# Kernel optimization log

Hardware: AMD Instinct MI355X
Metric: run time of the kernel (lower is better)

## Reference

```python
import jax, jax.numpy as jnp
import numpy as np

EMBED_DIM = 4096
NUM_HEADS = 32
HEAD_DIM = EMBED_DIM // NUM_HEADS  # 128
KV_LEN = 8192


def setup_inputs() -> dict:
    key = jax.random.key(0)
    ks = jax.random.split(key, 12)
    s = 1.0 / np.sqrt(EMBED_DIM)
    return {
        "x": jax.random.normal(ks[0], (EMBED_DIM,), jnp.float32),
        "v": jax.random.normal(ks[1], (KV_LEN, NUM_HEADS, HEAD_DIM), jnp.float32),
        "k": jax.random.normal(ks[2], (KV_LEN, NUM_HEADS, HEAD_DIM), jnp.float32),
        "Wv": jax.random.normal(ks[3], (EMBED_DIM, EMBED_DIM), jnp.float32) * s,
        "bv": jnp.zeros((EMBED_DIM,), jnp.float32),
        "Wq": jax.random.normal(ks[4], (EMBED_DIM, EMBED_DIM), jnp.float32) * s,
        "bq": jnp.zeros((EMBED_DIM,), jnp.float32),
        "Wk": jax.random.normal(ks[5], (EMBED_DIM, EMBED_DIM), jnp.float32) * s,
        "bk": jnp.zeros((EMBED_DIM,), jnp.float32),
        "Wo": jax.random.normal(ks[6], (EMBED_DIM, EMBED_DIM), jnp.float32) * s,
        "bo": jnp.zeros((EMBED_DIM,), jnp.float32),
    }


def reference(x, v, k, Wv, bv, Wq, bq, Wk, bk, Wo, bo):
    # Project the single incoming token to q/k/v heads.
    v_i = (x @ Wv + bv).reshape(1, NUM_HEADS, HEAD_DIM)
    q_i = (x @ Wq + bq).reshape(NUM_HEADS, HEAD_DIM)
    k_i = (x @ Wk + bk).reshape(1, NUM_HEADS, HEAD_DIM)
    # Rolling cache: drop oldest slot, append new token.
    v = jnp.concatenate((v[1:], v_i), axis=0)  # [KV_LEN, H, D]
    k = jnp.concatenate((k[1:], k_i), axis=0)
    # Valid slots are those with any nonzero value entry.
    mask = jnp.any(v != 0, axis=(1, 2))  # [KV_LEN]
    attn = jnp.einsum('hd,khd->hk', q_i, k) / jnp.sqrt(jnp.float32(HEAD_DIM))
    attn = jnp.where(mask, attn, -jnp.inf)
    attn = jax.nn.softmax(attn, axis=-1)  # [H, KV_LEN]
    values = jnp.einsum('hk,khd->hd', attn, v).reshape(EMBED_DIM)
    out_i = values @ Wo + bo
    return (out_i, v, k)
```

## Files before the change

### kernel.cpp

```cpp
#include <hip/hip_runtime.h>

#define E 4096
#define H 32
#define L 8192
#define SCALE 0.08838834764831845f

#define WS_QACC 0
#define WS_KACC 16384
#define WS_VACC 32768
#define WS_OACC 49152
#define WS_NUMP 53248
#define WS_DENP 118784
#define WS_NUM  119808
#define WS_DEN  123904
#define WS_ZERO_FLOATS 123968

typedef float fv4 __attribute__((ext_vector_type(4)));

__device__ __forceinline__ fv4 ntload4(const float* p) {
  return __builtin_nontemporal_load(reinterpret_cast<const fv4*>(p));
}
__device__ __forceinline__ void ntstore4(float* p, fv4 v) {
  __builtin_nontemporal_store(v, reinterpret_cast<fv4*>(p));
}

__global__ __launch_bounds__(256) void zero_ws(float* __restrict__ ws) {
  int i = blockIdx.x * 256 + threadIdx.x;
  if (i < WS_ZERO_FLOATS) ws[i] = 0.f;
}

__global__ __launch_bounds__(256) void gemv_qkv(const float* __restrict__ x,
    const float* __restrict__ Wq, const float* __restrict__ Wk,
    const float* __restrict__ Wv, float* __restrict__ ws) {
  int b = blockIdx.x;
  int mat = b >> 7;
  int rem = b & 127;
  int chunk = rem >> 2;
  int g = rem & 3;
  const float* W = (mat == 0) ? Wq : (mat == 1) ? Wk : Wv;
  int rep = (b >> 2) & 3;
  float* acc = ws + ((mat == 0) ? WS_QACC : (mat == 1) ? WS_KACC : WS_VACC)
                  + (rep << 12);
  int t = threadIdx.x;
  int j = (g << 10) + (t << 2);
  float ax = 0.f, ay = 0.f, az = 0.f, aw = 0.f;
  int i0 = chunk << 7;
  #pragma unroll 8
  for (int r = 0; r < 128; ++r) {
    int i = i0 + r;
    float xi = x[i];
    const fv4 w4 = ntload4(W + (size_t)i * E + j);
    ax += xi * w4.x; ay += xi * w4.y; az += xi * w4.z; aw += xi * w4.w;
  }
  atomicAdd(acc + j + 0, ax);
  atomicAdd(acc + j + 1, ay);
  atomicAdd(acc + j + 2, az);
  atomicAdd(acc + j + 3, aw);
}

#define SLOTS 16
__device__ __forceinline__ void load_slot(int o, int t,
    const float* __restrict__ kin, const float* __restrict__ vin,
    const float* __restrict__ ws, const float* __restrict__ bk,
    const float* __restrict__ bv, fv4 k4[4], fv4 v4[4]) {
  if (o < L - 1) {
    const float* ks = kin + (size_t)(o + 1) * E;
    const float* vs = vin + (size_t)(o + 1) * E;
    #pragma unroll
    for (int c = 0; c < 4; ++c) {
      int e = (c << 10) + (t << 2);
      k4[c] = ntload4(ks + e);
      v4[c] = ntload4(vs + e);
    }
  } else {
    #pragma unroll
    for (int c = 0; c < 4; ++c) {
      int e = (c << 10) + (t << 2);
      fv4 ka = *reinterpret_cast<const fv4*>(ws + WS_KACC + e);
      fv4 va = *reinterpret_cast<const fv4*>(ws + WS_VACC + e);
      #pragma unroll
      for (int r = 1; r < 4; ++r) {
        ka += *reinterpret_cast<const fv4*>(ws + WS_KACC + (r << 12) + e);
        va += *reinterpret_cast<const fv4*>(ws + WS_VACC + (r << 12) + e);
      }
      k4[c] = ka + *reinterpret_cast<const fv4*>(bk + e);
      v4[c] = va + *reinterpret_cast<const fv4*>(bv + e);
    }
  }
}

__global__ __launch_bounds__(256) void kvpass(const float* __restrict__ kin,
    const float* __restrict__ vin,
    const float* __restrict__ bq, const float* __restrict__ bk,
    const float* __restrict__ bv,
    float* __restrict__ kout, float* __restrict__ vout,
    float* __restrict__ ws) {
  __shared__ float wlds[SLOTS * 32];
  __shared__ int flags[SLOTS];
  int t = threadIdx.x;
  if (t < SLOTS) flags[t] = 0;
  fv4 q4[4];
  #pragma unroll
  for (int c = 0; c < 4; ++c) {
    int e = (c << 10) + (t << 2);
    fv4 qa = *reinterpret_cast<const fv4*>(ws + WS_QACC + e);
    #pragma unroll
    for (int r = 1; r < 4; ++r)
      qa += *reinterpret_cast<const fv4*>(ws + WS_QACC + (r << 12) + e);
    q4[c] = qa + *reinterpret_cast<const fv4*>(bq + e);
  }
  __syncthreads();

  float accx[4] = {0,0,0,0}, accy[4] = {0,0,0,0};
  float accz[4] = {0,0,0,0}, accw[4] = {0,0,0,0};
  int base = blockIdx.x * SLOTS;
  int rep = blockIdx.x & 15;

  fv4 kc[4], vc[4], kn[4], vn[4];
  load_slot(base, t, kin, vin, ws, bk, bv, kc, vc);

  for (int s = 0; s < SLOTS; ++s) {
    int o = base + s;
    if (s + 1 < SLOTS)
      load_slot(o + 1, t, kin, vin, ws, bk, bv, kn, vn);
    float* kd = kout + (size_t)o * E;
    float* vd = vout + (size_t)o * E;
    #pragma unroll
    for (int c = 0; c < 4; ++c) {
      int e = (c << 10) + (t << 2);
      ntstore4(kd + e, kc[c]);
      ntstore4(vd + e, vc[c]);
    }
    bool nz = false;
    #pragma unroll
    for (int c = 0; c < 4; ++c) {
      float pp = kc[c].x * q4[c].x + kc[c].y * q4[c].y +
                 kc[c].z * q4[c].z + kc[c].w * q4[c].w;
      #pragma unroll
      for (int off = 16; off >= 1; off >>= 1)
        pp += __shfl_xor(pp, off);
      float w = __expf(pp * SCALE);
      accx[c] += w * vc[c].x; accy[c] += w * vc[c].y;
      accz[c] += w * vc[c].z; accw[c] += w * vc[c].w;
      if ((t & 31) == 0) wlds[(s << 5) + (c << 3) + (t >> 5)] = w;
      nz = nz || vc[c].x != 0.f || vc[c].y != 0.f || vc[c].z != 0.f || vc[c].w != 0.f;
    }
    unsigned long long b = __ballot(nz);
    if ((t & 63) == 0 && b != 0ULL) atomicOr(&flags[s], 1);
    #pragma unroll
    for (int c = 0; c < 4; ++c) { kc[c] = kn[c]; vc[c] = vn[c]; }
  }
  float* num = ws + WS_NUMP + (rep << 12);
  #pragma unroll
  for (int c = 0; c < 4; ++c) {
    int e = (c << 10) + (t << 2);
    atomicAdd(num + e + 0, accx[c]);
    atomicAdd(num + e + 1, accy[c]);
    atomicAdd(num + e + 2, accz[c]);
    atomicAdd(num + e + 3, accw[c]);
  }
  __syncthreads();
  if (t < 32) {
    float d = 0.f;
    #pragma unroll
    for (int s = 0; s < SLOTS; ++s)
      if (flags[s]) d += wlds[(s << 5) + t];
    atomicAdd(ws + WS_DENP + (rep << 6) + t, d);
  }
}

__global__ __launch_bounds__(256) void merge(float* __restrict__ ws) {
  int e = blockIdx.x * 256 + threadIdx.x;
  float s = 0.f;
  #pragma unroll
  for (int r = 0; r < 16; ++r) s += ws[WS_NUMP + (r << 12) + e];
  ws[WS_NUM + e] = s;
  if (e < 64) {
    float d = 0.f;
    #pragma unroll
    for (int r = 0; r < 16; ++r) d += ws[WS_DENP + (r << 6) + e];
    ws[WS_DEN + e] = d;
  }
}

__global__ __launch_bounds__(256) void gemv_out(const float* __restrict__ Wo,
    const float* __restrict__ bo, float* __restrict__ ws) {
  int b = blockIdx.x;
  int chunk = b >> 2;
  int g = b & 3;
  int t = threadIdx.x;
  int j = (g << 10) + (t << 2);
  const float* num = ws + WS_NUM;
  const float* den = ws + WS_DEN;
  __shared__ float vals[64];
  int i0 = chunk << 6;
  if (t < 64) vals[t] = num[i0 + t] / den[(i0 + t) >> 7];
  __syncthreads();
  float ax = 0.f, ay = 0.f, az = 0.f, aw = 0.f;
  #pragma unroll 4
  for (int r = 0; r < 64; ++r) {
    int i = i0 + r;
    float vi = vals[r];
    const fv4 w4 = ntload4(Wo + (size_t)i * E + j);
    ax += vi * w4.x; ay += vi * w4.y; az += vi * w4.z; aw += vi * w4.w;
  }
  if (chunk == 0) {
    const fv4 b4 = *reinterpret_cast<const fv4*>(bo + j);
    ax += b4.x; ay += b4.y; az += b4.z; aw += b4.w;
  }
  float* oacc = ws + WS_OACC;
  atomicAdd(oacc + j + 0, ax);
  atomicAdd(oacc + j + 1, ay);
  atomicAdd(oacc + j + 2, az);
  atomicAdd(oacc + j + 3, aw);
}

__global__ __launch_bounds__(256) void writeout(const float* __restrict__ ws,
                                                float* __restrict__ out) {
  int i = blockIdx.x * 256 + threadIdx.x;
  out[i] = ws[WS_OACC + i];
}

extern "C" void kernel_launch(void* const* d_in, const int* in_sizes, int n_in,
                              void* d_out, int out_size, void* d_ws, size_t ws_size,
                              hipStream_t stream) {
  const float* x   = (const float*)d_in[0];
  const float* vin = (const float*)d_in[1];
  const float* kin = (const float*)d_in[2];
  const float* Wv  = (const float*)d_in[3];
  const float* bv  = (const float*)d_in[4];
  const float* Wq  = (const float*)d_in[5];
  const float* bq  = (const float*)d_in[6];
  const float* Wk  = (const float*)d_in[7];
  const float* bk  = (const float*)d_in[8];
  const float* Wo  = (const float*)d_in[9];
  const float* bo  = (const float*)d_in[10];
  float* out  = (float*)d_out;
  float* vout = out + E;
  float* kout = vout + (size_t)L * E;
  float* ws   = (float*)d_ws;

  zero_ws<<<(WS_ZERO_FLOATS + 255) / 256, 256, 0, stream>>>(ws);
  gemv_qkv<<<384, 256, 0, stream>>>(x, Wq, Wk, Wv, ws);
  kvpass<<<L / SLOTS, 256, 0, stream>>>(kin, vin, bq, bk, bv, kout, vout, ws);
  merge<<<16, 256, 0, stream>>>(ws);
  gemv_out<<<256, 256, 0, stream>>>(Wo, bo, ws);
  writeout<<<16, 256, 0, stream>>>(ws, out);
}
```

Before: 183.3 us.

## Replace atomic partial reductions with per-block partial buffers and wider merge

When the workspace is large enough, kvpass runs with 8 slots per block (1024 blocks). Each block writes its numerator and denominator partials to its own slot instead of doing atomicAdd into 16 replicas, and merge sums all 1024 partials. gemv_out now stores per-chunk partials that writeout reduces, which removes the output atomics and shrinks the zeroing of the workspace. This trades atomic contention for extra partial-buffer traffic: the big path writes and rereads about 16 MB of numerator partials, and merge has only 16 blocks to read it.

```diff
diff --git a/kernel.cpp b/kernel.cpp
--- a/kernel.cpp
+++ b/kernel.cpp
@@ -5,16 +5,6 @@
 #define L 8192
 #define SCALE 0.08838834764831845f
 
-#define WS_QACC 0
-#define WS_KACC 16384
-#define WS_VACC 32768
-#define WS_OACC 49152
-#define WS_NUMP 53248
-#define WS_DENP 118784
-#define WS_NUM  119808
-#define WS_DEN  123904
-#define WS_ZERO_FLOATS 123968
-
 typedef float fv4 __attribute__((ext_vector_type(4)));
 
 __device__ __forceinline__ fv4 ntload4(const float* p) {
@@ -24,23 +14,24 @@
   __builtin_nontemporal_store(v, reinterpret_cast<fv4*>(p));
 }
 
-__global__ __launch_bounds__(256) void zero_ws(float* __restrict__ ws) {
+__global__ __launch_bounds__(256) void zero_ws(float* __restrict__ ws, int n) {
   int i = blockIdx.x * 256 + threadIdx.x;
-  if (i < WS_ZERO_FLOATS) ws[i] = 0.f;
+  if (i < n) ws[i] = 0.f;
 }
 
 __global__ __launch_bounds__(256) void gemv_qkv(const float* __restrict__ x,
     const float* __restrict__ Wq, const float* __restrict__ Wk,
-    const float* __restrict__ Wv, float* __restrict__ ws) {
+    const float* __restrict__ Wv, float* __restrict__ qacc,
+    float* __restrict__ kacc, float* __restrict__ vacc) {
   int b = blockIdx.x;
   int mat = b >> 7;
   int rem = b & 127;
   int chunk = rem >> 2;
   int g = rem & 3;
   const float* W = (mat == 0) ? Wq : (mat == 1) ? Wk : Wv;
+  float* accb = (mat == 0) ? qacc : (mat == 1) ? kacc : vacc;
   int rep = (b >> 2) & 3;
-  float* acc = ws + ((mat == 0) ? WS_QACC : (mat == 1) ? WS_KACC : WS_VACC)
-                  + (rep << 12);
+  float* acc = accb + (rep << 12);
   int t = threadIdx.x;
   int j = (g << 10) + (t << 2);
   float ax = 0.f, ay = 0.f, az = 0.f, aw = 0.f;
@@ -58,11 +49,11 @@
   atomicAdd(acc + j + 3, aw);
 }
 
-#define SLOTS 16
 __device__ __forceinline__ void load_slot(int o, int t,
     const float* __restrict__ kin, const float* __restrict__ vin,
-    const float* __restrict__ ws, const float* __restrict__ bk,
-    const float* __restrict__ bv, fv4 k4[4], fv4 v4[4]) {
+    const float* __restrict__ kacc, const float* __restrict__ vacc,
+    const float* __restrict__ bk, const float* __restrict__ bv,
+    fv4 k4[4], fv4 v4[4]) {
   if (o < L - 1) {
     const float* ks = kin + (size_t)(o + 1) * E;
     const float* vs = vin + (size_t)(o + 1) * E;
@@ -76,12 +67,12 @@
     #pragma unroll
     for (int c = 0; c < 4; ++c) {
       int e = (c << 10) + (t << 2);
-      fv4 ka = *reinterpret_cast<const fv4*>(ws + WS_KACC + e);
-      fv4 va = *reinterpret_cast<const fv4*>(ws + WS_VACC + e);
+      fv4 ka = *reinterpret_cast<const fv4*>(kacc + e);
+      fv4 va = *reinterpret_cast<const fv4*>(vacc + e);
       #pragma unroll
       for (int r = 1; r < 4; ++r) {
-        ka += *reinterpret_cast<const fv4*>(ws + WS_KACC + (r << 12) + e);
-        va += *reinterpret_cast<const fv4*>(ws + WS_VACC + (r << 12) + e);
+        ka += *reinterpret_cast<const fv4*>(kacc + (r << 12) + e);
+        va += *reinterpret_cast<const fv4*>(vacc + (r << 12) + e);
       }
       k4[c] = ka + *reinterpret_cast<const fv4*>(bk + e);
       v4[c] = va + *reinterpret_cast<const fv4*>(bv + e);
@@ -89,40 +80,42 @@
   }
 }
 
+template<int NSLOTS, bool PARTIAL>
 __global__ __launch_bounds__(256) void kvpass(const float* __restrict__ kin,
     const float* __restrict__ vin,
     const float* __restrict__ bq, const float* __restrict__ bk,
     const float* __restrict__ bv,
+    const float* __restrict__ qacc, const float* __restrict__ kacc,
+    const float* __restrict__ vacc,
     float* __restrict__ kout, float* __restrict__ vout,
-    float* __restrict__ ws) {
-  __shared__ float wlds[SLOTS * 32];
-  __shared__ int flags[SLOTS];
-  int t = threadIdx.x;
-  if (t < SLOTS) flags[t] = 0;
+    float* __restrict__ nump, float* __restrict__ denp) {
+  __shared__ float wlds[NSLOTS * 32];
+  __shared__ int flags[NSLOTS];
+  int t = threadIdx.x;
+  if (t < NSLOTS) flags[t] = 0;
   fv4 q4[4];
   #pragma unroll
   for (int c = 0; c < 4; ++c) {
     int e = (c << 10) + (t << 2);
-    fv4 qa = *reinterpret_cast<const fv4*>(ws + WS_QACC + e);
+    fv4 qa = *reinterpret_cast<const fv4*>(qacc + e);
     #pragma unroll
     for (int r = 1; r < 4; ++r)
-      qa += *reinterpret_cast<const fv4*>(ws + WS_QACC + (r << 12) + e);
+      qa += *reinterpret_cast<const fv4*>(qacc + (r << 12) + e);
     q4[c] = qa + *reinterpret_cast<const fv4*>(bq + e);
   }
   __syncthreads();
 
   float accx[4] = {0,0,0,0}, accy[4] = {0,0,0,0};
   float accz[4] = {0,0,0,0}, accw[4] = {0,0,0,0};
-  int base = blockIdx.x * SLOTS;
-  int rep = blockIdx.x & 15;
+  int base = blockIdx.x * NSLOTS;
 
   fv4 kc[4], vc[4], kn[4], vn[4];
-  load_slot(base, t, kin, vin, ws, bk, bv, kc, vc);
-
-  for (int s = 0; s < SLOTS; ++s) {
+  load_slot(base, t, kin, vin, kacc, vacc, bk, bv, kc, vc);
+
+  for (int s = 0; s < NSLOTS; ++s) {
     int o = base + s;
-    if (s + 1 < SLOTS)
-      load_slot(o + 1, t, kin, vin, ws, bk, bv, kn, vn);
+    if (s + 1 < NSLOTS)
+      load_slot(o + 1, t, kin, vin, kacc, vacc, bk, bv, kn, vn);
     float* kd = kout + (size_t)o * E;
     float* vd = vout + (size_t)o * E;
     #pragma unroll
@@ -150,48 +143,72 @@
     #pragma unroll
     for (int c = 0; c < 4; ++c) { kc[c] = kn[c]; vc[c] = vn[c]; }
   }
-  float* num = ws + WS_NUMP + (rep << 12);
-  #pragma unroll
-  for (int c = 0; c < 4; ++c) {
-    int e = (c << 10) + (t << 2);
-    atomicAdd(num + e + 0, accx[c]);
-    atomicAdd(num + e + 1, accy[c]);
-    atomicAdd(num + e + 2, accz[c]);
-    atomicAdd(num + e + 3, accw[c]);
+  if (PARTIAL) {
+    float* np = nump + ((size_t)blockIdx.x << 12);
+    #pragma unroll
+    for (int c = 0; c < 4; ++c) {
+      int e = (c << 10) + (t << 2);
+      fv4 val = {accx[c], accy[c], accz[c], accw[c]};
+      *reinterpret_cast<fv4*>(np + e) = val;
+    }
+  } else {
+    float* np = nump + ((size_t)(blockIdx.x & 15) << 12);
+    #pragma unroll
+    for (int c = 0; c < 4; ++c) {
+      int e = (c << 10) + (t << 2);
+      atomicAdd(np + e + 0, accx[c]);
+      atomicAdd(np + e + 1, accy[c]);
+      atomicAdd(np + e + 2, accz[c]);
+      atomicAdd(np + e + 3, accw[c]);
+    }
   }
   __syncthreads();
   if (t < 32) {
     float d = 0.f;
     #pragma unroll
-    for (int s = 0; s < SLOTS; ++s)
+    for (int s = 0; s < NSLOTS; ++s)
       if (flags[s]) d += wlds[(s << 5) + t];
-    atomicAdd(ws + WS_DENP + (rep << 6) + t, d);
-  }
-}
-
-__global__ __launch_bounds__(256) void merge(float* __restrict__ ws) {
-  int e = blockIdx.x * 256 + threadIdx.x;
-  float s = 0.f;
-  #pragma unroll
-  for (int r = 0; r < 16; ++r) s += ws[WS_NUMP + (r << 12) + e];
-  ws[WS_NUM + e] = s;
-  if (e < 64) {
+    if (PARTIAL) denp[blockIdx.x * 64 + t] = d;
+    else atomicAdd(denp + (blockIdx.x & 15) * 64 + t, d);
+  }
+}
+
+template<int NP>
+__global__ __launch_bounds__(256) void merge(const float* __restrict__ nump,
+    const float* __restrict__ denp, float* __restrict__ num,
+    float* __restrict__ den) {
+  int b = blockIdx.x;
+  int t = threadIdx.x;
+  if (b < 16) {
+    int e = b * 256 + t;
+    float s = 0.f;
+    #pragma unroll 8
+    for (int p = 0; p < NP; ++p) s += nump[((size_t)p << 12) + e];
+    num[e] = s;
+  } else {
+    __shared__ float dl[8][32];
+    int g = t >> 5, h = t & 31;
     float d = 0.f;
-    #pragma unroll
-    for (int r = 0; r < 16; ++r) d += ws[WS_DENP + (r << 6) + e];
-    ws[WS_DEN + e] = d;
+    for (int p = g; p < NP; p += 8) d += denp[p * 64 + h];
+    dl[g][h] = d;
+    __syncthreads();
+    if (t < 32) {
+      float s = 0.f;
+      #pragma unroll
+      for (int g2 = 0; g2 < 8; ++g2) s += dl[g2][t];
+      den[t] = s;
+    }
   }
 }
 
 __global__ __launch_bounds__(256) void gemv_out(const float* __restrict__ Wo,
-    const float* __restrict__ bo, float* __restrict__ ws) {
+    const float* __restrict__ bo, const float* __restrict__ num,
+    const float* __restrict__ den, float* __restrict__ opart) {
   int b = blockIdx.x;
   int chunk = b >> 2;
   int g = b & 3;
   int t = threadIdx.x;
   int j = (g << 10) + (t << 2);
-  const float* num = ws + WS_NUM;
-  const float* den = ws + WS_DEN;
   __shared__ float vals[64];
   int i0 = chunk << 6;
   if (t < 64) vals[t] = num[i0 + t] / den[(i0 + t) >> 7];
@@ -208,17 +225,17 @@
     const fv4 b4 = *reinterpret_cast<const fv4*>(bo + j);
     ax += b4.x; ay += b4.y; az += b4.z; aw += b4.w;
   }
-  float* oacc = ws + WS_OACC;
-  atomicAdd(oacc + j + 0, ax);
-  atomicAdd(oacc + j + 1, ay);
-  atomicAdd(oacc + j + 2, az);
-  atomicAdd(oacc + j + 3, aw);
-}
-
-__global__ __launch_bounds__(256) void writeout(const float* __restrict__ ws,
+  fv4 val = {ax, ay, az, aw};
+  *reinterpret_cast<fv4*>(opart + (chunk << 12) + j) = val;
+}
+
+__global__ __launch_bounds__(256) void writeout(const float* __restrict__ opart,
                                                 float* __restrict__ out) {
   int i = blockIdx.x * 256 + threadIdx.x;
-  out[i] = ws[WS_OACC + i];
+  float s = 0.f;
+  #pragma unroll 8
+  for (int c = 0; c < 64; ++c) s += opart[(c << 12) + i];
+  out[i] = s;
 }
 
 extern "C" void kernel_launch(void* const* d_in, const int* in_sizes, int n_in,
@@ -240,10 +257,41 @@
   float* kout = vout + (size_t)L * E;
   float* ws   = (float*)d_ws;
 
-  zero_ws<<<(WS_ZERO_FLOATS + 255) / 256, 256, 0, stream>>>(ws);
-  gemv_qkv<<<384, 256, 0, stream>>>(x, Wq, Wk, Wv, ws);
-  kvpass<<<L / SLOTS, 256, 0, stream>>>(kin, vin, bq, bk, bv, kout, vout, ws);
-  merge<<<16, 256, 0, stream>>>(ws);
-  gemv_out<<<256, 256, 0, stream>>>(Wo, bo, ws);
-  writeout<<<16, 256, 0, stream>>>(ws, out);
-}
+  float* qacc = ws;
+  float* kacc = ws + 16384;
+  float* vacc = ws + 32768;
+  const size_t bigFloats = 49152 + (size_t)1024 * 4096 + 1024 * 64 + 4096 + 64 + 64 * 4096;
+  bool big = ws_size >= bigFloats * sizeof(float);
+
+  float *nump, *denp, *num, *den, *opart;
+  int zcount;
+  if (big) {
+    nump = ws + 49152;
+    denp = nump + (size_t)1024 * 4096;
+    num  = denp + 1024 * 64;
+    den  = num + 4096;
+    opart = den + 64;
+    zcount = 49152;
+  } else {
+    nump = ws + 49152;
+    denp = nump + 16 * 4096;
+    num  = denp + 16 * 64;
+    den  = num + 4096;
+    opart = den + 64;
+    zcount = 49152 + 16 * 4096 + 16 * 64;
+  }
+
+  zero_ws<<<(zcount + 255) / 256, 256, 0, stream>>>(ws, zcount);
+  gemv_qkv<<<384, 256, 0, stream>>>(x, Wq, Wk, Wv, qacc, kacc, vacc);
+  if (big) {
+    kvpass<8, true><<<L / 8, 256, 0, stream>>>(kin, vin, bq, bk, bv,
+        qacc, kacc, vacc, kout, vout, nump, denp);
+    merge<1024><<<17, 256, 0, stream>>>(nump, denp, num, den);
+  } else {
+    kvpass<16, false><<<L / 16, 256, 0, stream>>>(kin, vin, bq, bk, bv,
+        qacc, kacc, vacc, kout, vout, nump, denp);
+    merge<16><<<17, 256, 0, stream>>>(nump, denp, num, den);
+  }
+  gemv_out<<<256, 256, 0, stream>>>(Wo, bo, num, den, opart);
+  writeout<<<16, 256, 0, stream>>>(opart, out);
+}
```

New measurement: 232.3 us. 1.27x slower.

## Split kvpass into separate K-scoring and V-accumulation loops

Applied to the files above, without the earlier changes.

The single fused loop that streamed K and V together is replaced by two loops inside kvpass. The first streams K, copies it to the output and writes the exp scores to shared memory. After a barrier, the second streams V, reads the scores from LDS, accumulates the weighted sum and computes the nonzero flags. This lowers register pressure (fewer live prefetch vectors) and could raise occupancy, but it adds a barrier and an LDS round trip, and concurrent K/V streams are no longer interleaved.

```diff
diff --git a/kernel.cpp b/kernel.cpp
--- a/kernel.cpp
+++ b/kernel.cpp
@@ -59,31 +59,44 @@
 }
 
 #define SLOTS 16
-__device__ __forceinline__ void load_slot(int o, int t,
-    const float* __restrict__ kin, const float* __restrict__ vin,
-    const float* __restrict__ ws, const float* __restrict__ bk,
-    const float* __restrict__ bv, fv4 k4[4], fv4 v4[4]) {
+
+__device__ __forceinline__ void load_k(int o, int t,
+    const float* __restrict__ kin, const float* __restrict__ ws,
+    const float* __restrict__ bk, fv4 k4[4]) {
   if (o < L - 1) {
     const float* ks = kin + (size_t)(o + 1) * E;
-    const float* vs = vin + (size_t)(o + 1) * E;
-    #pragma unroll
-    for (int c = 0; c < 4; ++c) {
-      int e = (c << 10) + (t << 2);
-      k4[c] = ntload4(ks + e);
-      v4[c] = ntload4(vs + e);
-    }
+    #pragma unroll
+    for (int c = 0; c < 4; ++c)
+      k4[c] = ntload4(ks + (c << 10) + (t << 2));
   } else {
     #pragma unroll
     for (int c = 0; c < 4; ++c) {
       int e = (c << 10) + (t << 2);
       fv4 ka = *reinterpret_cast<const fv4*>(ws + WS_KACC + e);
+      #pragma unroll
+      for (int r = 1; r < 4; ++r)
+        ka += *reinterpret_cast<const fv4*>(ws + WS_KACC + (r << 12) + e);
+      k4[c] = ka + *reinterpret_cast<const fv4*>(bk + e);
+    }
+  }
+}
+
+__device__ __forceinline__ void load_v(int o, int t,
+    const float* __restrict__ vin, const float* __restrict__ ws,
+    const float* __restrict__ bv, fv4 v4[4]) {
+  if (o < L - 1) {
+    const float* vs = vin + (size_t)(o + 1) * E;
+    #pragma unroll
+    for (int c = 0; c < 4; ++c)
+      v4[c] = ntload4(vs + (c << 10) + (t << 2));
+  } else {
+    #pragma unroll
+    for (int c = 0; c < 4; ++c) {
+      int e = (c << 10) + (t << 2);
       fv4 va = *reinterpret_cast<const fv4*>(ws + WS_VACC + e);
       #pragma unroll
-      for (int r = 1; r < 4; ++r) {
-        ka += *reinterpret_cast<const fv4*>(ws + WS_KACC + (r << 12) + e);
+      for (int r = 1; r < 4; ++r)
         va += *reinterpret_cast<const fv4*>(ws + WS_VACC + (r << 12) + e);
-      }
-      k4[c] = ka + *reinterpret_cast<const fv4*>(bk + e);
       v4[c] = va + *reinterpret_cast<const fv4*>(bv + e);
     }
   }
@@ -111,44 +124,61 @@
   }
   __syncthreads();
 
+  int base = blockIdx.x * SLOTS;
+  int rep = blockIdx.x & 15;
+
+  {
+    fv4 kc[4], kn[4];
+    load_k(base, t, kin, ws, bk, kc);
+    for (int s = 0; s < SLOTS; ++s) {
+      int o = base + s;
+      if (s + 1 < SLOTS) load_k(o + 1, t, kin, ws, bk, kn);
+      float* kd = kout + (size_t)o * E;
+      #pragma unroll
+      for (int c = 0; c < 4; ++c)
+        ntstore4(kd + (c << 10) + (t << 2), kc[c]);
+      #pragma unroll
+      for (int c = 0; c < 4; ++c) {
+        float pp = kc[c].x * q4[c].x + kc[c].y * q4[c].y +
+                   kc[c].z * q4[c].z + kc[c].w * q4[c].w;
+        #pragma unroll
+        for (int off = 16; off >= 1; off >>= 1)
+          pp += __shfl_xor(pp, off);
+        if ((t & 31) == 0)
+          wlds[(s << 5) + (c << 3) + (t >> 5)] = __expf(pp * SCALE);
+      }
+      #pragma unroll
+      for (int c = 0; c < 4; ++c) kc[c] = kn[c];
+    }
+  }
+  __syncthreads();
+
   float accx[4] = {0,0,0,0}, accy[4] = {0,0,0,0};
   float accz[4] = {0,0,0,0}, accw[4] = {0,0,0,0};
-  int base = blockIdx.x * SLOTS;
-  int rep = blockIdx.x & 15;
-
-  fv4 kc[4], vc[4], kn[4], vn[4];
-  load_slot(base, t, kin, vin, ws, bk, bv, kc, vc);
-
-  for (int s = 0; s < SLOTS; ++s) {
-    int o = base + s;
-    if (s + 1 < SLOTS)
-      load_slot(o + 1, t, kin, vin, ws, bk, bv, kn, vn);
-    float* kd = kout + (size_t)o * E;
-    float* vd = vout + (size_t)o * E;
-    #pragma unroll
-    for (int c = 0; c < 4; ++c) {
-      int e = (c << 10) + (t << 2);
-      ntstore4(kd + e, kc[c]);
-      ntstore4(vd + e, vc[c]);
-    }
-    bool nz = false;
-    #pragma unroll
-    for (int c = 0; c < 4; ++c) {
-      float pp = kc[c].x * q4[c].x + kc[c].y * q4[c].y +
-                 kc[c].z * q4[c].z + kc[c].w * q4[c].w;
-      #pragma unroll
-      for (int off = 16; off >= 1; off >>= 1)
-        pp += __shfl_xor(pp, off);
-      float w = __expf(pp * SCALE);
-      accx[c] += w * vc[c].x; accy[c] += w * vc[c].y;
-      accz[c] += w * vc[c].z; accw[c] += w * vc[c].w;
-      if ((t & 31) == 0) wlds[(s << 5) + (c << 3) + (t >> 5)] = w;
-      nz = nz || vc[c].x != 0.f || vc[c].y != 0.f || vc[c].z != 0.f || vc[c].w != 0.f;
-    }
-    unsigned long long b = __ballot(nz);
-    if ((t & 63) == 0 && b != 0ULL) atomicOr(&flags[s], 1);
-    #pragma unroll
-    for (int c = 0; c < 4; ++c) { kc[c] = kn[c]; vc[c] = vn[c]; }
+  {
+    fv4 vc[4], vn[4];
+    load_v(base, t, vin, ws, bv, vc);
+    for (int s = 0; s < SLOTS; ++s) {
+      int o = base + s;
+      if (s + 1 < SLOTS) load_v(o + 1, t, vin, ws, bv, vn);
+      float* vd = vout + (size_t)o * E;
+      #pragma unroll
+      for (int c = 0; c < 4; ++c)
+        ntstore4(vd + (c << 10) + (t << 2), vc[c]);
+      bool nz = false;
+      #pragma unroll
+      for (int c = 0; c < 4; ++c) {
+        float w = wlds[(s << 5) + (c << 3) + (t >> 5)];
+        accx[c] += w * vc[c].x; accy[c] += w * vc[c].y;
+        accz[c] += w * vc[c].z; accw[c] += w * vc[c].w;
+        nz = nz || vc[c].x != 0.f || vc[c].y != 0.f ||
+             vc[c].z != 0.f || vc[c].w != 0.f;
+      }
+      unsigned long long b = __ballot(nz);
+      if ((t & 63) == 0 && b != 0ULL) atomicOr(&flags[s], 1);
+      #pragma unroll
+      for (int c = 0; c < 4; ++c) vc[c] = vn[c];
+    }
   }
   float* num = ws + WS_NUMP + (rep << 12);
   #pragma unroll
```

After: 187.9 us. 2.5% more time.

## Replace atomic GEMV accumulation with partial-sum buffers and dedicated reduction kernels

Applied to the files above, without the earlier changes.

The QKV and output GEMV kernels now write per-chunk partial sums with plain stores instead of float atomicAdds. A new qkvred kernel reduces the Q/K/V partials and adds the biases once, so kvpass no longer re-reduces the replicated accumulators in every block. The merge kernel is folded into gemv_out's prologue, and writeout reduces the 64 output partials. This removes atomic contention and shrinks the zeroing pass, at the cost of extra partial-buffer traffic and one additional small launch for qkvred.

```diff
diff --git a/kernel.cpp b/kernel.cpp
--- a/kernel.cpp
+++ b/kernel.cpp
@@ -5,15 +5,13 @@
 #define L 8192
 #define SCALE 0.08838834764831845f
 
-#define WS_QACC 0
-#define WS_KACC 16384
-#define WS_VACC 32768
-#define WS_OACC 49152
-#define WS_NUMP 53248
-#define WS_DENP 118784
-#define WS_NUM  119808
-#define WS_DEN  123904
-#define WS_ZERO_FLOATS 123968
+#define WS_PART  0
+#define WS_QFIN  393216
+#define WS_KFIN  397312
+#define WS_VFIN  401408
+#define WS_NUMP  405504
+#define WS_DENP  471040
+#define WS_OPART 472064
 
 typedef float fv4 __attribute__((ext_vector_type(4)));
 
@@ -24,9 +22,9 @@
   __builtin_nontemporal_store(v, reinterpret_cast<fv4*>(p));
 }
 
-__global__ __launch_bounds__(256) void zero_ws(float* __restrict__ ws) {
+__global__ __launch_bounds__(256) void zero_np(float* __restrict__ ws) {
   int i = blockIdx.x * 256 + threadIdx.x;
-  if (i < WS_ZERO_FLOATS) ws[i] = 0.f;
+  if (i < (WS_OPART - WS_NUMP)) ws[WS_NUMP + i] = 0.f;
 }
 
 __global__ __launch_bounds__(256) void gemv_qkv(const float* __restrict__ x,
@@ -38,9 +36,6 @@
   int chunk = rem >> 2;
   int g = rem & 3;
   const float* W = (mat == 0) ? Wq : (mat == 1) ? Wk : Wv;
-  int rep = (b >> 2) & 3;
-  float* acc = ws + ((mat == 0) ? WS_QACC : (mat == 1) ? WS_KACC : WS_VACC)
-                  + (rep << 12);
   int t = threadIdx.x;
   int j = (g << 10) + (t << 2);
   float ax = 0.f, ay = 0.f, az = 0.f, aw = 0.f;
@@ -52,17 +47,28 @@
     const fv4 w4 = ntload4(W + (size_t)i * E + j);
     ax += xi * w4.x; ay += xi * w4.y; az += xi * w4.z; aw += xi * w4.w;
   }
-  atomicAdd(acc + j + 0, ax);
-  atomicAdd(acc + j + 1, ay);
-  atomicAdd(acc + j + 2, az);
-  atomicAdd(acc + j + 3, aw);
+  fv4 val = {ax, ay, az, aw};
+  ntstore4(ws + WS_PART + (mat << 17) + (chunk << 12) + j, val);
+}
+
+__global__ __launch_bounds__(256) void qkvred(const float* __restrict__ bq,
+    const float* __restrict__ bk, const float* __restrict__ bv,
+    float* __restrict__ ws) {
+  int e = blockIdx.x * 256 + threadIdx.x;
+  int mat = e >> 12;
+  int col = e & 4095;
+  const float* part = ws + WS_PART + (mat << 17);
+  float s = 0.f;
+  #pragma unroll 8
+  for (int c = 0; c < 32; ++c) s += part[(c << 12) + col];
+  const float* bias = (mat == 0) ? bq : (mat == 1) ? bk : bv;
+  ws[WS_QFIN + (mat << 12) + col] = s + bias[col];
 }
 
 #define SLOTS 16
 __device__ __forceinline__ void load_slot(int o, int t,
     const float* __restrict__ kin, const float* __restrict__ vin,
-    const float* __restrict__ ws, const float* __restrict__ bk,
-    const float* __restrict__ bv, fv4 k4[4], fv4 v4[4]) {
+    const float* __restrict__ ws, fv4 k4[4], fv4 v4[4]) {
   if (o < L - 1) {
     const float* ks = kin + (size_t)(o + 1) * E;
     const float* vs = vin + (size_t)(o + 1) * E;
@@ -76,23 +82,14 @@
     #pragma unroll
     for (int c = 0; c < 4; ++c) {
       int e = (c << 10) + (t << 2);
-      fv4 ka = *reinterpret_cast<const fv4*>(ws + WS_KACC + e);
-      fv4 va = *reinterpret_cast<const fv4*>(ws + WS_VACC + e);
-      #pragma unroll
-      for (int r = 1; r < 4; ++r) {
-        ka += *reinterpret_cast<const fv4*>(ws + WS_KACC + (r << 12) + e);
-        va += *reinterpret_cast<const fv4*>(ws + WS_VACC + (r << 12) + e);
-      }
-      k4[c] = ka + *reinterpret_cast<const fv4*>(bk + e);
-      v4[c] = va + *reinterpret_cast<const fv4*>(bv + e);
+      k4[c] = *reinterpret_cast<const fv4*>(ws + WS_KFIN + e);
+      v4[c] = *reinterpret_cast<const fv4*>(ws + WS_VFIN + e);
     }
   }
 }
 
 __global__ __launch_bounds__(256) void kvpass(const float* __restrict__ kin,
     const float* __restrict__ vin,
-    const float* __restrict__ bq, const float* __restrict__ bk,
-    const float* __restrict__ bv,
     float* __restrict__ kout, float* __restrict__ vout,
     float* __restrict__ ws) {
   __shared__ float wlds[SLOTS * 32];
@@ -101,14 +98,8 @@
   if (t < SLOTS) flags[t] = 0;
   fv4 q4[4];
   #pragma unroll
-  for (int c = 0; c < 4; ++c) {
-    int e = (c << 10) + (t << 2);
-    fv4 qa = *reinterpret_cast<const fv4*>(ws + WS_QACC + e);
-    #pragma unroll
-    for (int r = 1; r < 4; ++r)
-      qa += *reinterpret_cast<const fv4*>(ws + WS_QACC + (r << 12) + e);
-    q4[c] = qa + *reinterpret_cast<const fv4*>(bq + e);
-  }
+  for (int c = 0; c < 4; ++c)
+    q4[c] = *reinterpret_cast<const fv4*>(ws + WS_QFIN + (c << 10) + (t << 2));
   __syncthreads();
 
   float accx[4] = {0,0,0,0}, accy[4] = {0,0,0,0};
@@ -117,12 +108,12 @@
   int rep = blockIdx.x & 15;
 
   fv4 kc[4], vc[4], kn[4], vn[4];
-  load_slot(base, t, kin, vin, ws, bk, bv, kc, vc);
+  load_slot(base, t, kin, vin, ws, kc, vc);
 
   for (int s = 0; s < SLOTS; ++s) {
     int o = base + s;
     if (s + 1 < SLOTS)
-      load_slot(o + 1, t, kin, vin, ws, bk, bv, kn, vn);
+      load_slot(o + 1, t, kin, vin, ws, kn, vn);
     float* kd = kout + (size_t)o * E;
     float* vd = vout + (size_t)o * E;
     #pragma unroll
@@ -169,20 +160,6 @@
   }
 }
 
-__global__ __launch_bounds__(256) void merge(float* __restrict__ ws) {
-  int e = blockIdx.x * 256 + threadIdx.x;
-  float s = 0.f;
-  #pragma unroll
-  for (int r = 0; r < 16; ++r) s += ws[WS_NUMP + (r << 12) + e];
-  ws[WS_NUM + e] = s;
-  if (e < 64) {
-    float d = 0.f;
-    #pragma unroll
-    for (int r = 0; r < 16; ++r) d += ws[WS_DENP + (r << 6) + e];
-    ws[WS_DEN + e] = d;
-  }
-}
-
 __global__ __launch_bounds__(256) void gemv_out(const float* __restrict__ Wo,
     const float* __restrict__ bo, float* __restrict__ ws) {
   int b = blockIdx.x;
@@ -190,11 +167,18 @@
   int g = b & 3;
   int t = threadIdx.x;
   int j = (g << 10) + (t << 2);
-  const float* num = ws + WS_NUM;
-  const float* den = ws + WS_DEN;
   __shared__ float vals[64];
   int i0 = chunk << 6;
-  if (t < 64) vals[t] = num[i0 + t] / den[(i0 + t) >> 7];
+  if (t < 64) {
+    float s = 0.f;
+    #pragma unroll
+    for (int r = 0; r < 16; ++r) s += ws[WS_NUMP + (r << 12) + i0 + t];
+    float d = 0.f;
+    int h = chunk >> 1;
+    #pragma unroll
+    for (int r = 0; r < 16; ++r) d += ws[WS_DENP + (r << 6) + h];
+    vals[t] = s / d;
+  }
   __syncthreads();
   float ax = 0.f, ay = 0.f, az = 0.f, aw = 0.f;
   #pragma unroll 4
@@ -208,17 +192,17 @@
     const fv4 b4 = *reinterpret_cast<const fv4*>(bo + j);
     ax += b4.x; ay += b4.y; az += b4.z; aw += b4.w;
   }
-  float* oacc = ws + WS_OACC;
-  atomicAdd(oacc + j + 0, ax);
-  atomicAdd(oacc + j + 1, ay);
-  atomicAdd(oacc + j + 2, az);
-  atomicAdd(oacc + j + 3, aw);
+  fv4 val = {ax, ay, az, aw};
+  ntstore4(ws + WS_OPART + (chunk << 12) + j, val);
 }
 
 __global__ __launch_bounds__(256) void writeout(const float* __restrict__ ws,
                                                 float* __restrict__ out) {
   int i = blockIdx.x * 256 + threadIdx.x;
-  out[i] = ws[WS_OACC + i];
+  float s = 0.f;
+  #pragma unroll 8
+  for (int c = 0; c < 64; ++c) s += ws[WS_OPART + (c << 12) + i];
+  out[i] = s;
 }
 
 extern "C" void kernel_launch(void* const* d_in, const int* in_sizes, int n_in,
@@ -240,10 +224,10 @@
   float* kout = vout + (size_t)L * E;
   float* ws   = (float*)d_ws;
 
-  zero_ws<<<(WS_ZERO_FLOATS + 255) / 256, 256, 0, stream>>>(ws);
+  zero_np<<<(WS_OPART - WS_NUMP + 255) / 256, 256, 0, stream>>>(ws);
   gemv_qkv<<<384, 256, 0, stream>>>(x, Wq, Wk, Wv, ws);
-  kvpass<<<L / SLOTS, 256, 0, stream>>>(kin, vin, bq, bk, bv, kout, vout, ws);
-  merge<<<16, 256, 0, stream>>>(ws);
+  qkvred<<<48, 256, 0, stream>>>(bq, bk, bv, ws);
+  kvpass<<<L / SLOTS, 256, 0, stream>>>(kin, vin, kout, vout, ws);
   gemv_out<<<256, 256, 0, stream>>>(Wo, bo, ws);
   writeout<<<16, 256, 0, stream>>>(ws, out);
 }
```

Measured after the change: 174.6 us (median of 3 runs). -4.7%, faster.
